# Kernel tuning notes

Hardware: AMD Instinct MI355X
Metric: run time of the kernel (lower is better)

The kernel has to match this reference:

```python
import jax, jax.numpy as jnp
import numpy as np

B, S, D, H = 4, 2048, 1024, 16
HD = D // H

def setup_inputs() -> dict:
    key = jax.random.key(0)
    ks = jax.random.split(key, 11)
    scale = 1.0 / np.sqrt(D)
    return {
        "query": jax.random.normal(ks[0], (B, S, D), jnp.float32),
        "key_": jax.random.normal(ks[1], (B, S, D), jnp.float32),
        "value": jax.random.normal(ks[2], (B, S, D), jnp.float32),
        "wq": jax.random.normal(ks[3], (D, D), jnp.float32) * scale,
        "bq": jnp.zeros((D,), jnp.float32),
        "wk": jax.random.normal(ks[4], (D, D), jnp.float32) * scale,
        "bk": jnp.zeros((D,), jnp.float32),
        "wv": jax.random.normal(ks[5], (D, D), jnp.float32) * scale,
        "bv": jnp.zeros((D,), jnp.float32),
        "wo": jax.random.normal(ks[6], (D, D), jnp.float32) * scale,
        "bo": jnp.zeros((D,), jnp.float32),
    }

def _split_heads(x):
    b, s, _ = x.shape
    return x.reshape(b, s, H, HD).transpose(0, 2, 1, 3)  # [B,H,S,HD]

def reference(query, key_, value, wq, bq, wk, bk, wv, bv, wo, bo):
    q = _split_heads(query @ wq + bq)
    k = _split_heads(key_ @ wk + bk)
    v = _split_heads(value @ wv + bv)
    scores = jnp.einsum('bhqd,bhkd->bhqk', q, k) / jnp.sqrt(jnp.float32(HD))
    attn = jax.nn.softmax(scores, axis=-1)
    ctx = jnp.einsum('bhqk,bhkd->bhqd', attn, v)
    ctx = ctx.transpose(0, 2, 1, 3).reshape(B, S, D)
    return ctx @ wo + bo
```

## Files before the change

kernel.cpp:

```cpp
#include <hip/hip_runtime.h>

typedef _Float16 f16;
typedef _Float16 f16x8 __attribute__((ext_vector_type(8)));
typedef _Float16 f16x4 __attribute__((ext_vector_type(4)));
typedef float    f32x4 __attribute__((ext_vector_type(4)));
typedef float    f32x16 __attribute__((ext_vector_type(16)));

#define MROWS 8192
#define KDIM  1024
#define SEQ   2048
#define HDIM  64
#define QKV_LD 3072

#if __has_builtin(__builtin_amdgcn_exp2f)
#define EXP2(x) __builtin_amdgcn_exp2f(x)
#else
#define EXP2(x) exp2f(x)
#endif

#define AS1 __attribute__((address_space(1)))
#define AS3 __attribute__((address_space(3)))

__device__ __forceinline__ int swz5(int row) { return (row ^ (row >> 3)) & 7; }

__global__ __launch_bounds__(256) void cast3_k(const float* __restrict__ a,
                                               const float* __restrict__ b,
                                               const float* __restrict__ c,
                                               f16* __restrict__ out) {
  int i = blockIdx.x * 256 + threadIdx.x;
  const float* src = (blockIdx.y == 0) ? a : (blockIdx.y == 1) ? b : c;
  float4 v = ((const float4*)src)[i];
  f16x4 o = { (f16)v.x, (f16)v.y, (f16)v.z, (f16)v.w };
  *(f16x4*)&out[(size_t)blockIdx.y * 8388608 + (size_t)i * 4] = o;
}

__global__ __launch_bounds__(256) void transpose_cast_k(const float* __restrict__ w,
                                                        f16* __restrict__ wt) {
  __shared__ float t[32][33];
  int tx = threadIdx.x, ty = threadIdx.y;
  int bx = blockIdx.x * 32, by = blockIdx.y * 32;
  #pragma unroll
  for (int i = ty; i < 32; i += 8) t[i][tx] = w[(size_t)(by + i) * KDIM + bx + tx];
  __syncthreads();
  #pragma unroll
  for (int i = ty; i < 32; i += 8) wt[(size_t)(bx + i) * KDIM + by + tx] = (f16)t[tx][i];
}

__global__ __launch_bounds__(256) void concat3_k(const float* __restrict__ a,
                                                 const float* __restrict__ b,
                                                 const float* __restrict__ c,
                                                 float* __restrict__ o) {
  int i = blockIdx.x * 256 + threadIdx.x;
  float v;
  if (i < 1024) v = a[i]; else if (i < 2048) v = b[i - 1024]; else v = c[i - 2048];
  o[i] = v;
}

template<bool OUT_F16>
__global__ __launch_bounds__(256) void gemm_k(const f16* __restrict__ A0, size_t aStride,
                                              const f16* __restrict__ Bt,
                                              const float* __restrict__ bias,
                                              void* __restrict__ Cout, int ldc) {
  __shared__ f16 sA[128 * 64];
  __shared__ f16 sB[128 * 64];
  const int tid  = threadIdx.x;
  const int lane = tid & 63;
  const int r    = lane & 15;
  const int q    = lane >> 4;
  const int wave = tid >> 6;
  const int m0 = blockIdx.x * 128;
  const int ng = blockIdx.z * 1024 + blockIdx.y * 128;
  const int wm = (wave >> 1) * 64;
  const int wn = (wave & 1) * 64;
  const f16* A = A0 + (size_t)blockIdx.z * aStride;

  f32x4 acc[4][4];
  #pragma unroll
  for (int i = 0; i < 4; ++i)
    #pragma unroll
    for (int j = 0; j < 4; ++j) acc[i][j] = (f32x4){0.f, 0.f, 0.f, 0.f};

  for (int kt = 0; kt < KDIM; kt += 64) {
    #pragma unroll
    for (int issue = 0; issue < 4; ++issue) {
      int g   = issue * 256 + tid;
      int row = g >> 3;
      int csw = (g & 7) ^ (row & 7);
      const f16* gA = A  + (size_t)(m0 + row) * KDIM + kt + csw * 8;
      const f16* gB = Bt + (size_t)(ng + row) * KDIM + kt + csw * 8;
      int lb = __builtin_amdgcn_readfirstlane((issue * 256 + (tid & ~63)) * 16);
      __builtin_amdgcn_global_load_lds((const AS1 void*)gA,
                                       (AS3 void*)((char*)sA + lb), 16, 0, 0);
      __builtin_amdgcn_global_load_lds((const AS1 void*)gB,
                                       (AS3 void*)((char*)sB + lb), 16, 0, 0);
    }
    __syncthreads();
    #pragma unroll
    for (int kk = 0; kk < 64; kk += 32) {
      f16x8 af[4], bf[4];
      #pragma unroll
      for (int mi = 0; mi < 4; ++mi) {
        int row = wm + mi * 16 + r;
        int cs  = ((kk >> 3) + q) ^ (row & 7);
        af[mi] = *(const f16x8*)&sA[row * 64 + cs * 8];
      }
      #pragma unroll
      for (int ni = 0; ni < 4; ++ni) {
        int row = wn + ni * 16 + r;
        int cs  = ((kk >> 3) + q) ^ (row & 7);
        bf[ni] = *(const f16x8*)&sB[row * 64 + cs * 8];
      }
      #pragma unroll
      for (int mi = 0; mi < 4; ++mi)
        #pragma unroll
        for (int ni = 0; ni < 4; ++ni)
          acc[mi][ni] = __builtin_amdgcn_mfma_f32_16x16x32_f16(af[mi], bf[ni], acc[mi][ni], 0, 0, 0);
    }
    __syncthreads();
  }
  #pragma unroll
  for (int ni = 0; ni < 4; ++ni) {
    int col = ng + wn + ni * 16 + r;
    float bv = bias[col];
    #pragma unroll
    for (int mi = 0; mi < 4; ++mi) {
      int rowb = m0 + wm + mi * 16 + q * 4;
      #pragma unroll
      for (int reg = 0; reg < 4; ++reg) {
        float v = acc[mi][ni][reg] + bv;
        if constexpr (OUT_F16) ((f16*)Cout)[(size_t)(rowb + reg) * ldc + col] = (f16)v;
        else                   ((float*)Cout)[(size_t)(rowb + reg) * ldc + col] = v;
      }
    }
  }
}

__global__ __launch_bounds__(512, 2) void gemm256_k(const f16* __restrict__ A0,
                                                    const f16* __restrict__ Bt,
                                                    const float* __restrict__ bias,
                                                    f16* __restrict__ Cout) {
  __shared__ f16 smem[65536];
  const int tid  = threadIdx.x;
  const int lane = tid & 63;
  const int r    = lane & 15;
  const int q    = lane >> 4;
  const int wave = tid >> 6;
  const int wm   = wave >> 2;
  const int wn   = wave & 3;

  const int id  = blockIdx.x;
  const int swz = (id & 7) * 48 + (id >> 3);
  const int bx  = swz & 31;
  const int by  = swz >> 5;
  const int m0  = bx * 256;
  const int n0  = by * 256;
  const f16* A  = A0 + (size_t)(by >> 2) * 8388608;

  const int srow0 = tid >> 3;
  const int srow1 = (512 + tid) >> 3;
  const int sg0 = (tid & 7) ^ (srow0 & 7);
  const int sg1 = (tid & 7) ^ (srow1 & 7);
  const f16* gA0 = A  + (size_t)(m0 + srow0) * KDIM + sg0 * 8;
  const f16* gA1 = A  + (size_t)(m0 + srow1) * KDIM + sg1 * 8;
  const f16* gB0 = Bt + (size_t)(n0 + srow0) * KDIM + sg0 * 8;
  const f16* gB1 = Bt + (size_t)(n0 + srow1) * KDIM + sg1 * 8;
  const int lb0 = __builtin_amdgcn_readfirstlane((tid & ~63) * 16);
  const int lb1 = __builtin_amdgcn_readfirstlane((512 + (tid & ~63)) * 16);

  auto issueA = [&](int s, int hi) {
    char* base = (char*)smem + (s & 1) * 65536 + hi * 16384;
    const f16* s0 = gA0 + (size_t)hi * (128 * KDIM) + s * 64;
    const f16* s1 = gA1 + (size_t)hi * (128 * KDIM) + s * 64;
    __builtin_amdgcn_global_load_lds((const AS1 void*)s0, (AS3 void*)(base + lb0), 16, 0, 0);
    __builtin_amdgcn_global_load_lds((const AS1 void*)s1, (AS3 void*)(base + lb1), 16, 0, 0);
  };
  auto issueB = [&](int s, int hi) {
    char* base = (char*)smem + (s & 1) * 65536 + 32768 + hi * 16384;
    const f16* s0 = gB0 + (size_t)hi * (128 * KDIM) + s * 64;
    const f16* s1 = gB1 + (size_t)hi * (128 * KDIM) + s * 64;
    __builtin_amdgcn_global_load_lds((const AS1 void*)s0, (AS3 void*)(base + lb0), 16, 0, 0);
    __builtin_amdgcn_global_load_lds((const AS1 void*)s1, (AS3 void*)(base + lb1), 16, 0, 0);
  };

  auto readA = [&](int s, int qa, f16x8 (&af)[4][2]) {
    const f16* rg = smem + (s & 1) * 32768 + qa * 8192;
    #pragma unroll
    for (int mi = 0; mi < 4; ++mi) {
      int rl = wm * 64 + mi * 16 + r;
      #pragma unroll
      for (int kk2 = 0; kk2 < 2; ++kk2) {
        int g = kk2 * 4 + q;
        af[mi][kk2] = *(const f16x8*)&rg[rl * 64 + ((g ^ (rl & 7)) * 8)];
      }
    }
  };
  auto readB = [&](int s, int qb, f16x8 (&bf)[2][2]) {
    const f16* rg = smem + (s & 1) * 32768 + 16384 + qb * 8192;
    #pragma unroll
    for (int ni = 0; ni < 2; ++ni) {
      int rl = wn * 32 + ni * 16 + r;
      #pragma unroll
      for (int kk2 = 0; kk2 < 2; ++kk2) {
        int g = kk2 * 4 + q;
        bf[ni][kk2] = *(const f16x8*)&rg[rl * 64 + ((g ^ (rl & 7)) * 8)];
      }
    }
  };

  f32x4 acc[8][4];
  #pragma unroll
  for (int i = 0; i < 8; ++i)
    #pragma unroll
    for (int j = 0; j < 4; ++j) acc[i][j] = (f32x4){0.f, 0.f, 0.f, 0.f};

  auto mmaQ = [&](f16x8 (&af)[4][2], f16x8 (&bf)[2][2], int qa, int qb) {
    __builtin_amdgcn_s_setprio(1);
    #pragma unroll
    for (int kk2 = 0; kk2 < 2; ++kk2)
      #pragma unroll
      for (int mi = 0; mi < 4; ++mi)
        #pragma unroll
        for (int ni = 0; ni < 2; ++ni)
          acc[qa * 4 + mi][qb * 2 + ni] =
            __builtin_amdgcn_mfma_f32_16x16x32_f16(af[mi][kk2], bf[ni][kk2],
                                                   acc[qa * 4 + mi][qb * 2 + ni], 0, 0, 0);
    __builtin_amdgcn_s_setprio(0);
  };

  auto bar = [] {
    __builtin_amdgcn_sched_barrier(0);
    __builtin_amdgcn_s_barrier();
    __builtin_amdgcn_sched_barrier(0);
  };

  issueA(0, 0); issueB(0, 0); issueB(0, 1); issueA(0, 1);
  issueB(1, 0); issueA(1, 0); issueB(1, 1);
  asm volatile("s_waitcnt vmcnt(6)");
  bar();

  f16x8 alo[4][2], ahi[4][2], blo[2][2], bhi[2][2];
  #pragma unroll 1
  for (int s = 0; s < 16; ++s) {
    readA(s, 0, alo);
    readB(s, 0, blo);
    if (s + 1 < 16) issueA(s + 1, 1);
    bar();
    mmaQ(alo, blo, 0, 0);
    bar();
    readB(s, 1, bhi);
    if (s + 2 < 16) issueB(s + 2, 0);
    bar();
    mmaQ(alo, bhi, 0, 1);
    bar();
    readA(s, 1, ahi);
    if (s + 2 < 16) issueA(s + 2, 0);
    bar();
    mmaQ(ahi, bhi, 1, 1);
    bar();
    if (s + 2 < 16) issueB(s + 2, 1);
    if (s < 14)       { asm volatile("s_waitcnt vmcnt(6)"); }
    else if (s == 14) { asm volatile("s_waitcnt vmcnt(0)"); }
    bar();
    mmaQ(ahi, blo, 1, 0);
    bar();
  }

  #pragma unroll
  for (int mi8 = 0; mi8 < 8; ++mi8) {
    int rowb = m0 + (mi8 >> 2) * 128 + wm * 64 + (mi8 & 3) * 16 + q * 4;
    #pragma unroll
    for (int ni4 = 0; ni4 < 4; ++ni4) {
      int col = n0 + (ni4 >> 1) * 128 + wn * 32 + (ni4 & 1) * 16 + r;
      float bv = bias[col];
      #pragma unroll
      for (int reg = 0; reg < 4; ++reg)
        Cout[(size_t)(rowb + reg) * QKV_LD + col] = (f16)(acc[mi8][ni4][reg] + bv);
    }
  }
}

__global__ __launch_bounds__(256) void vtrans_k(const f16* __restrict__ qkv,
                                                f16* __restrict__ vt) {
  __shared__ f16 t[64 * 64];
  const int tid = threadIdx.x;
  const int st = blockIdx.x, h = blockIdx.y, b = blockIdx.z;
  const f16* src = qkv + (size_t)(b * SEQ + st * 64) * QKV_LD + 2048 + h * HDIM;
  #pragma unroll
  for (int issue = 0; issue < 2; ++issue) {
    int g = issue * 256 + tid;
    int srow = g >> 3, c = g & 7;
    f16x8 v = *(const f16x8*)(src + (size_t)srow * QKV_LD + c * 8);
    *(f16x8*)&t[srow * 64 + (c ^ (srow & 7)) * 8] = v;
  }
  __syncthreads();
  f16* dst = vt + (size_t)(b * 16 + h) * HDIM * SEQ + st * 64;
  #pragma unroll
  for (int issue = 0; issue < 2; ++issue) {
    int g = issue * 256 + tid;
    int d = g >> 3, c8 = g & 7;
    f16x8 o;
    #pragma unroll
    for (int j = 0; j < 8; ++j) {
      int s = c8 * 8 + j;
      o[j] = t[s * 64 + ((d >> 3) ^ (s & 7)) * 8 + (d & 7)];
    }
    *(f16x8*)(dst + (size_t)d * SEQ + c8 * 8) = o;
  }
}

__global__ __launch_bounds__(256) void attn_k(const f16* __restrict__ qkv,
                                              const f16* __restrict__ vt,
                                              f16* __restrict__ ctx) {
  __shared__ f16 smem[16384];
  const int tid  = threadIdx.x;
  const int lane = tid & 63;
  const int wave = tid >> 6;
  const int n    = lane & 31;
  const int q32  = lane >> 5;
  const int flat = blockIdx.x + (blockIdx.y << 4) + (blockIdx.z << 8);
  const int qt = flat >> 6;
  const int h  = flat & 15;
  const int b  = (flat >> 4) & 3;

  const f16* Qb  = qkv + (size_t)b * SEQ * QKV_LD + h * HDIM;
  const f16* Vtb = vt + (size_t)(b * 16 + h) * HDIM * SEQ;
  const int qrow = qt * 128 + wave * 32 + n;

  f16x8 qf[4];
  {
    const f16* qp = Qb + (size_t)qrow * QKV_LD + q32 * 8;
    const f16 sc = (f16)(0.125f * 1.44269504f);
    #pragma unroll
    for (int cc = 0; cc < 4; ++cc) qf[cc] = *(const f16x8*)(qp + cc * 16) * sc;
  }

  const int r0 = tid >> 3, c0 = tid & 7;
  const f16* gK0 = Qb + 1024 + (size_t)r0 * QKV_LD + (c0 ^ swz5(r0)) * 8;
  const f16* gK1 = Qb + 1024 + (size_t)(r0 + 32) * QKV_LD + (c0 ^ swz5(r0 + 32)) * 8;
  const f16* gV0 = Vtb + (size_t)r0 * SEQ + (c0 ^ swz5(r0)) * 8;
  const f16* gV1 = Vtb + (size_t)(r0 + 32) * SEQ + (c0 ^ swz5(r0 + 32)) * 8;
  const int lb = __builtin_amdgcn_readfirstlane((tid & ~63) * 16);

  auto stage = [&](int bufbyte) {
    char* base = (char*)smem + bufbyte + lb;
    __builtin_amdgcn_global_load_lds((const AS1 void*)gK0, (AS3 void*)(base), 16, 0, 0);
    __builtin_amdgcn_global_load_lds((const AS1 void*)gK1, (AS3 void*)(base + 4096), 16, 0, 0);
    __builtin_amdgcn_global_load_lds((const AS1 void*)gV0, (AS3 void*)(base + 8192), 16, 0, 0);
    __builtin_amdgcn_global_load_lds((const AS1 void*)gV1, (AS3 void*)(base + 12288), 16, 0, 0);
    gK0 += 64 * QKV_LD; gK1 += 64 * QKV_LD; gV0 += 64; gV1 += 64;
  };

  f32x16 ot[2];
  #pragma unroll
  for (int db = 0; db < 2; ++db)
    #pragma unroll
    for (int i = 0; i < 16; ++i) ot[db][i] = 0.f;
  float ls = 0.f;

  auto compute = [&](int bufe) {
    const f16* sK = smem + bufe;
    const f16* sV = smem + bufe + 4096;
    f16x4 p[2][4];
    #pragma unroll
    for (int kc = 0; kc < 2; ++kc) {
      f32x16 st;
      #pragma unroll
      for (int i = 0; i < 16; ++i) st[i] = -2.8853901817f;
      __builtin_amdgcn_s_setprio(1);
      #pragma unroll
      for (int cc = 0; cc < 4; ++cc) {
        int row = kc * 32 + n;
        f16x8 kf = *(const f16x8*)&sK[row * 64 + (((cc * 2 + q32) ^ swz5(row)) * 8)];
        st = __builtin_amdgcn_mfma_f32_32x32x16_f16(kf, qf[cc], st, 0, 0, 0);
      }
      __builtin_amdgcn_s_setprio(0);
      #pragma unroll
      for (int g = 0; g < 4; ++g) {
        float e0 = EXP2(st[4 * g + 0]);
        float e1 = EXP2(st[4 * g + 1]);
        float e2 = EXP2(st[4 * g + 2]);
        float e3 = EXP2(st[4 * g + 3]);
        ls += (e0 + e1) + (e2 + e3);
        p[kc][g] = (f16x4){ (f16)e0, (f16)e1, (f16)e2, (f16)e3 };
      }
    }
    __builtin_amdgcn_s_setprio(1);
    #pragma unroll
    for (int db = 0; db < 2; ++db) {
      int row = db * 32 + n;
      int fr = swz5(row);
      const f16* vrow = &sV[row * 64];
      #pragma unroll
      for (int cc = 0; cc < 4; ++cc) {
        int hg = (2 * cc) ^ fr;
        f16x4 vlo = *(const f16x4*)&vrow[hg * 8 + q32 * 4];
        f16x4 vhi = *(const f16x4*)&vrow[(hg ^ 1) * 8 + q32 * 4];
        f16x8 vf = __builtin_shufflevector(vlo, vhi, 0, 1, 2, 3, 4, 5, 6, 7);
        f16x8 pf = __builtin_shufflevector(p[cc >> 1][2 * (cc & 1)],
                                           p[cc >> 1][2 * (cc & 1) + 1],
                                           0, 1, 2, 3, 4, 5, 6, 7);
        ot[db] = __builtin_amdgcn_mfma_f32_32x32x16_f16(vf, pf, ot[db], 0, 0, 0);
      }
    }
    __builtin_amdgcn_s_setprio(0);
  };

  stage(0);
  #pragma unroll 1
  for (int it = 0; it < 32; it += 2) {
    __syncthreads();
    stage(16384);
    compute(0);
    __syncthreads();
    if (it + 2 < 32) stage(0);
    compute(8192);
  }

  ls += __shfl_xor(ls, 32);
  float inv = 1.0f / ls;

  f16* sO = smem;
  int nl = wave * 32 + n;
  int fo = swz5(nl);
  #pragma unroll
  for (int db = 0; db < 2; ++db)
    #pragma unroll
    for (int g = 0; g < 4; ++g) {
      f16x4 o = { (f16)(ot[db][4 * g + 0] * inv), (f16)(ot[db][4 * g + 1] * inv),
                  (f16)(ot[db][4 * g + 2] * inv), (f16)(ot[db][4 * g + 3] * inv) };
      *(f16x4*)&sO[nl * 64 + (((db * 4 + g) ^ fo) * 8) + q32 * 4] = o;
    }
  __syncthreads();
  #pragma unroll
  for (int issue = 0; issue < 4; ++issue) {
    int g = issue * 256 + tid;
    int rr = g >> 3, sg = g & 7;
    f16x8 v = *(const f16x8*)&sO[rr * 64 + ((sg ^ swz5(rr)) * 8)];
    *(f16x8*)&ctx[(size_t)(b * SEQ + qt * 128 + rr) * KDIM + h * HDIM + sg * 8] = v;
  }
}

extern "C" void kernel_launch(void* const* d_in, const int* in_sizes, int n_in,
                              void* d_out, int out_size, void* d_ws, size_t ws_size,
                              hipStream_t stream) {
  (void)in_sizes; (void)n_in; (void)out_size; (void)ws_size;
  const float* query = (const float*)d_in[0];
  const float* key_  = (const float*)d_in[1];
  const float* value = (const float*)d_in[2];
  const float* wq = (const float*)d_in[3];
  const float* bq = (const float*)d_in[4];
  const float* wk = (const float*)d_in[5];
  const float* bk = (const float*)d_in[6];
  const float* wv = (const float*)d_in[7];
  const float* bv = (const float*)d_in[8];
  const float* wo = (const float*)d_in[9];
  const float* bo = (const float*)d_in[10];
  float* out = (float*)d_out;

  char* ws = (char*)d_ws;
  f16*   X16  = (f16*)(ws);
  f16*   qkvT = (f16*)(ws + 50331648);
  f16*   woT  = (f16*)(ws + 56623104);
  float* b3   = (float*)(ws + 58720256);
  f16*   QKV  = (f16*)(ws + 58736640);
  f16*   ctx  = (f16*)(ws);
  f16*   Vt   = (f16*)(ws + 16777216);

  cast3_k<<<dim3(8192, 3), 256, 0, stream>>>(query, key_, value, X16);
  transpose_cast_k<<<dim3(32, 32), dim3(32, 8), 0, stream>>>(wq, qkvT);
  transpose_cast_k<<<dim3(32, 32), dim3(32, 8), 0, stream>>>(wk, qkvT + 1048576);
  transpose_cast_k<<<dim3(32, 32), dim3(32, 8), 0, stream>>>(wv, qkvT + 2097152);
  transpose_cast_k<<<dim3(32, 32), dim3(32, 8), 0, stream>>>(wo, woT);
  concat3_k<<<12, 256, 0, stream>>>(bq, bk, bv, b3);

  gemm256_k<<<dim3(384), 512, 0, stream>>>(X16, qkvT, b3, QKV);
  vtrans_k<<<dim3(32, 16, 4), 256, 0, stream>>>(QKV, Vt);
  attn_k<<<dim3(16, 16, 4), 256, 0, stream>>>(QKV, Vt, ctx);
  gemm_k<false><<<dim3(64, 8, 1), 256, 0, stream>>>(ctx, (size_t)0, woT, bo, (void*)out, 1024);
}
```

Measured before the change: 363.1 us.

## Double attention query tile to 256 rows with 512 threads; merge weight transposes

The attention kernel now uses 512-thread blocks covering 256 query rows. The K/V tile loaded into shared memory is shared by twice as many waves, so each thread issues half as many async global-to-LDS loads and total K/V traffic halves. A barrier is added before the output staging reuses shared memory. The four weight transpose launches are also merged into a single launch with a z dimension. The trade-off is half as many attention blocks (512) and larger per-block synchronization cost, which could hurt latency hiding.

```diff
diff --git a/kernel.cpp b/kernel.cpp
--- a/kernel.cpp
+++ b/kernel.cpp
@@ -34,9 +34,16 @@
   *(f16x4*)&out[(size_t)blockIdx.y * 8388608 + (size_t)i * 4] = o;
 }
 
-__global__ __launch_bounds__(256) void transpose_cast_k(const float* __restrict__ w,
-                                                        f16* __restrict__ wt) {
+__global__ __launch_bounds__(256) void wtrans4_k(const float* __restrict__ w0,
+                                                 const float* __restrict__ w1,
+                                                 const float* __restrict__ w2,
+                                                 const float* __restrict__ w3,
+                                                 f16* __restrict__ qkvT,
+                                                 f16* __restrict__ woT) {
   __shared__ float t[32][33];
+  const int z = blockIdx.z;
+  const float* w = (z == 0) ? w0 : (z == 1) ? w1 : (z == 2) ? w2 : w3;
+  f16* wt = (z == 3) ? woT : (qkvT + z * 1048576);
   int tx = threadIdx.x, ty = threadIdx.y;
   int bx = blockIdx.x * 32, by = blockIdx.y * 32;
   #pragma unroll
@@ -308,23 +315,24 @@
   }
 }
 
-__global__ __launch_bounds__(256) void attn_k(const f16* __restrict__ qkv,
-                                              const f16* __restrict__ vt,
-                                              f16* __restrict__ ctx) {
+__global__ __launch_bounds__(512, 4) void attn_k(const f16* __restrict__ qkv,
+                                                 const f16* __restrict__ vt,
+                                                 f16* __restrict__ ctx) {
   __shared__ f16 smem[16384];
   const int tid  = threadIdx.x;
   const int lane = tid & 63;
   const int wave = tid >> 6;
   const int n    = lane & 31;
   const int q32  = lane >> 5;
-  const int flat = blockIdx.x + (blockIdx.y << 4) + (blockIdx.z << 8);
+  const int flat = blockIdx.x + (blockIdx.y << 3) + (blockIdx.z << 7);
   const int qt = flat >> 6;
-  const int h  = flat & 15;
-  const int b  = (flat >> 4) & 3;
+  const int hb = flat & 63;
+  const int h  = hb & 15;
+  const int b  = hb >> 4;
 
   const f16* Qb  = qkv + (size_t)b * SEQ * QKV_LD + h * HDIM;
   const f16* Vtb = vt + (size_t)(b * 16 + h) * HDIM * SEQ;
-  const int qrow = qt * 128 + wave * 32 + n;
+  const int qrow = qt * 256 + wave * 32 + n;
 
   f16x8 qf[4];
   {
@@ -336,18 +344,14 @@
 
   const int r0 = tid >> 3, c0 = tid & 7;
   const f16* gK0 = Qb + 1024 + (size_t)r0 * QKV_LD + (c0 ^ swz5(r0)) * 8;
-  const f16* gK1 = Qb + 1024 + (size_t)(r0 + 32) * QKV_LD + (c0 ^ swz5(r0 + 32)) * 8;
   const f16* gV0 = Vtb + (size_t)r0 * SEQ + (c0 ^ swz5(r0)) * 8;
-  const f16* gV1 = Vtb + (size_t)(r0 + 32) * SEQ + (c0 ^ swz5(r0 + 32)) * 8;
   const int lb = __builtin_amdgcn_readfirstlane((tid & ~63) * 16);
 
   auto stage = [&](int bufbyte) {
     char* base = (char*)smem + bufbyte + lb;
     __builtin_amdgcn_global_load_lds((const AS1 void*)gK0, (AS3 void*)(base), 16, 0, 0);
-    __builtin_amdgcn_global_load_lds((const AS1 void*)gK1, (AS3 void*)(base + 4096), 16, 0, 0);
     __builtin_amdgcn_global_load_lds((const AS1 void*)gV0, (AS3 void*)(base + 8192), 16, 0, 0);
-    __builtin_amdgcn_global_load_lds((const AS1 void*)gV1, (AS3 void*)(base + 12288), 16, 0, 0);
-    gK0 += 64 * QKV_LD; gK1 += 64 * QKV_LD; gV0 += 64; gV1 += 64;
+    gK0 += 64 * QKV_LD; gV0 += 64;
   };
 
   f32x16 ot[2];
@@ -419,6 +423,7 @@
   ls += __shfl_xor(ls, 32);
   float inv = 1.0f / ls;
 
+  __syncthreads();
   f16* sO = smem;
   int nl = wave * 32 + n;
   int fo = swz5(nl);
@@ -433,10 +438,10 @@
   __syncthreads();
   #pragma unroll
   for (int issue = 0; issue < 4; ++issue) {
-    int g = issue * 256 + tid;
+    int g = issue * 512 + tid;
     int rr = g >> 3, sg = g & 7;
     f16x8 v = *(const f16x8*)&sO[rr * 64 + ((sg ^ swz5(rr)) * 8)];
-    *(f16x8*)&ctx[(size_t)(b * SEQ + qt * 128 + rr) * KDIM + h * HDIM + sg * 8] = v;
+    *(f16x8*)&ctx[(size_t)(b * SEQ + qt * 256 + rr) * KDIM + h * HDIM + sg * 8] = v;
   }
 }
 
@@ -467,14 +472,11 @@
   f16*   Vt   = (f16*)(ws + 16777216);
 
   cast3_k<<<dim3(8192, 3), 256, 0, stream>>>(query, key_, value, X16);
-  transpose_cast_k<<<dim3(32, 32), dim3(32, 8), 0, stream>>>(wq, qkvT);
-  transpose_cast_k<<<dim3(32, 32), dim3(32, 8), 0, stream>>>(wk, qkvT + 1048576);
-  transpose_cast_k<<<dim3(32, 32), dim3(32, 8), 0, stream>>>(wv, qkvT + 2097152);
-  transpose_cast_k<<<dim3(32, 32), dim3(32, 8), 0, stream>>>(wo, woT);
+  wtrans4_k<<<dim3(32, 32, 4), dim3(32, 8), 0, stream>>>(wq, wk, wv, wo, qkvT, woT);
   concat3_k<<<12, 256, 0, stream>>>(bq, bk, bv, b3);
 
   gemm256_k<<<dim3(384), 512, 0, stream>>>(X16, qkvT, b3, QKV);
   vtrans_k<<<dim3(32, 16, 4), 256, 0, stream>>>(QKV, Vt);
-  attn_k<<<dim3(16, 16, 4), 256, 0, stream>>>(QKV, Vt, ctx);
+  attn_k<<<dim3(8, 16, 4), 512, 0, stream>>>(QKV, Vt, ctx);
   gemm_k<false><<<dim3(64, 8, 1), 256, 0, stream>>>(ctx, (size_t)0, woT, bo, (void*)out, 1024);
 }
```

New measurement: 377.0 us. 3.8% more time.
